# Performance work log

Measured on AMD Instinct MI355X. Metric: run time of the kernel, lower is better.

## Reference

```python
import jax, jax.numpy as jnp
import numpy as np

D_MODEL = 1024
N_HEADS = 16
D_FF = 4096
EPS = 1e-6


def layernorm(x, alpha, bias):
    # torch.std uses Bessel correction (ddof=1)
    mean = jnp.mean(x, axis=-1, keepdims=True)
    std = jnp.std(x, axis=-1, keepdims=True, ddof=1)
    return alpha * (x - mean) / (std + EPS) + bias


def setup_inputs() -> dict:
    key = jax.random.key(0)
    ks = jax.random.split(key, 12)
    s = 1.0 / np.sqrt(D_MODEL)
    sf = 1.0 / np.sqrt(D_FF)
    return {
        "x": jax.random.normal(ks[0], (2, 2048, D_MODEL), jnp.float32),
        "mask": jnp.ones((2, 1, 1, 2048), jnp.int32),
        "wq": jax.random.normal(ks[1], (D_MODEL, D_MODEL), jnp.float32) * s,
        "wk": jax.random.normal(ks[2], (D_MODEL, D_MODEL), jnp.float32) * s,
        "wv": jax.random.normal(ks[3], (D_MODEL, D_MODEL), jnp.float32) * s,
        "wo": jax.random.normal(ks[4], (D_MODEL, D_MODEL), jnp.float32) * s,
        "wo_b": jnp.zeros((D_MODEL,), jnp.float32),
        "w1": jax.random.normal(ks[5], (D_MODEL, D_FF), jnp.float32) * s,
        "b1": jnp.zeros((D_FF,), jnp.float32),
        "w2": jax.random.normal(ks[6], (D_FF, D_MODEL), jnp.float32) * sf,
        "b2": jnp.zeros((D_MODEL,), jnp.float32),
        "alpha1": jnp.ones((D_MODEL,), jnp.float32),
        "bias1": jnp.zeros((D_MODEL,), jnp.float32),
        "alpha2": jnp.ones((D_MODEL,), jnp.float32),
        "bias2": jnp.zeros((D_MODEL,), jnp.float32),
    }


def reference(x, mask, wq, wk, wv, wo, wo_b, w1, b1, w2, b2,
              alpha1, bias1, alpha2, bias2):
    B, S, D = x.shape
    h, dk = N_HEADS, D_MODEL // N_HEADS
    # projections -> [B, h, S, dk]
    q = (x @ wq).reshape(B, S, h, dk).transpose(0, 2, 1, 3)
    k = (x @ wk).reshape(B, S, h, dk).transpose(0, 2, 1, 3)
    v = (x @ wv).reshape(B, S, h, dk).transpose(0, 2, 1, 3)
    scores = jnp.einsum('bhqd,bhkd->bhqk', q, k) / jnp.sqrt(jnp.float32(dk))
    scores = jnp.where(mask == 0, jnp.float32(-1e9), scores)
    attn = jax.nn.softmax(scores, axis=-1)
    ctx = jnp.einsum('bhqk,bhkd->bhqd', attn, v)
    ctx = ctx.transpose(0, 2, 1, 3).reshape(B, S, D)
    attn_out = ctx @ wo + wo_b
    x = layernorm(x + attn_out, alpha1, bias1)
    ff = jax.nn.relu(x @ w1 + b1) @ w2 + b2
    x = layernorm(x + ff, alpha2, bias2)
    return x
```

## Files before the change

### kernel.cpp

```cpp
#include <hip/hip_runtime.h>
#include <hip/hip_bf16.h>

#define D_MODEL 1024
#define N_HEADS 16
#define DK      64
#define SEQ     2048
#define BATCH   2
#define D_FF    4096
#define ROWS    (BATCH*SEQ)
#define LN_EPS  1e-6f
#define KTILE   128

typedef __hip_bfloat16 bf16;
typedef __attribute__((ext_vector_type(8))) short frag8;
typedef __attribute__((ext_vector_type(4))) float facc4;

__device__ inline float bf2f(unsigned short u){ return __uint_as_float(((unsigned)u) << 16); }
__device__ inline float toF(bf16 v){ return __bfloat162float(v); }
__device__ inline unsigned short f2bu(float f){ bf16 h = __float2bfloat16(f); return *reinterpret_cast<unsigned short*>(&h); }

__device__ inline float ld1(const void* p, size_t idx, bool f32) {
    return f32 ? ((const float*)p)[idx] : toF(((const bf16*)p)[idx]);
}

struct U8 { unsigned short v[8]; };
__device__ inline U8 ld8bf(const void* p, size_t idx, bool f32) {
    U8 r;
    if (!f32) {
        *reinterpret_cast<uint4*>(r.v) = *reinterpret_cast<const uint4*>((const unsigned short*)p + idx);
    } else {
        const float* f = (const float*)p + idx;
        const float4 a = *reinterpret_cast<const float4*>(f);
        const float4 b = *reinterpret_cast<const float4*>(f + 4);
        r.v[0]=f2bu(a.x); r.v[1]=f2bu(a.y); r.v[2]=f2bu(a.z); r.v[3]=f2bu(a.w);
        r.v[4]=f2bu(b.x); r.v[5]=f2bu(b.y); r.v[6]=f2bu(b.z); r.v[7]=f2bu(b.w);
    }
    return r;
}

__device__ inline void gld16(const void* g, void* l) {
    __builtin_amdgcn_global_load_lds(
        reinterpret_cast<const __attribute__((address_space(1))) void*>(
            reinterpret_cast<uintptr_t>(g)),
        reinterpret_cast<__attribute__((address_space(3))) void*>(
            (unsigned int)reinterpret_cast<uintptr_t>(l)),
        16, 0, 0);
}

__global__ void probe_kernel(const void* __restrict__ xp, int* __restrict__ flag) {
    __shared__ int hit;
    if (threadIdx.x == 0) hit = 0;
    __syncthreads();
    const bf16* p = (const bf16*)xp;
    int bad = 0;
    for (int i = threadIdx.x; i < 8192; i += 256) {
        float v = fabsf(toF(p[i]));
        if (!(v <= 1e5f)) bad = 1;
    }
    if (bad) atomicOr(&hit, 1);
    __syncthreads();
    if (threadIdx.x == 0) *flag = hit;
}

__global__ __launch_bounds__(256) void xcvt_kernel(const void* __restrict__ x,
    bf16* __restrict__ out, const int* __restrict__ flagp)
{
    const bool f32 = (*flagp) != 0;
    const size_t i = ((size_t)blockIdx.x * 256 + threadIdx.x) * 8;
    U8 d = ld8bf(x, i, f32);
    *reinterpret_cast<uint4*>(out + i) = *reinterpret_cast<const uint4*>(d.v);
}

__global__ __launch_bounds__(256) void transpose_kernel(const void* __restrict__ W,
    bf16* __restrict__ WT, int K, int N, const int* __restrict__ flagp)
{
    const bool f32 = (*flagp) != 0;
    __shared__ float tile[32][33];
    const int tx = threadIdx.x, ty = threadIdx.y;
    const int n0 = blockIdx.x * 32, k0 = blockIdx.y * 32;
    #pragma unroll
    for (int r = 0; r < 4; ++r)
        tile[ty + 8*r][tx] = ld1(W, (size_t)(k0 + ty + 8*r) * N + n0 + tx, f32);
    __syncthreads();
    #pragma unroll
    for (int r = 0; r < 4; ++r)
        WT[(size_t)(n0 + ty + 8*r) * K + k0 + tx] = __float2bfloat16(tile[tx][ty + 8*r]);
}

__global__ __launch_bounds__(256) void transpose4_kernel(const void* __restrict__ w0,
    const void* __restrict__ w1, const void* __restrict__ w2, const void* __restrict__ w3,
    bf16* __restrict__ WT4, const int* __restrict__ flagp)
{
    const bool f32 = (*flagp) != 0;
    const int which = blockIdx.z;
    const void* W = (which == 0) ? w0 : (which == 1) ? w1 : (which == 2) ? w2 : w3;
    bf16* WT = WT4 + (size_t)which * D_MODEL * D_MODEL;
    __shared__ float tile[32][33];
    const int tx = threadIdx.x, ty = threadIdx.y;
    const int n0 = blockIdx.x * 32, k0 = blockIdx.y * 32;
    #pragma unroll
    for (int r = 0; r < 4; ++r)
        tile[ty + 8*r][tx] = ld1(W, (size_t)(k0 + ty + 8*r) * D_MODEL + n0 + tx, f32);
    __syncthreads();
    #pragma unroll
    for (int r = 0; r < 4; ++r)
        WT[(size_t)(n0 + ty + 8*r) * D_MODEL + k0 + tx] = __float2bfloat16(tile[tx][ty + 8*r]);
}

__global__ __launch_bounds__(256) void vtrans_kernel(const bf16* __restrict__ V,
    bf16* __restrict__ VT)
{
    __shared__ unsigned short tile[32][33];
    const int tx = threadIdx.x, ty = threadIdx.y;
    const int s0 = blockIdx.x * 32, d0 = blockIdx.y * 32;
    const int bh = blockIdx.z, b = bh >> 4, h = bh & 15;
    #pragma unroll
    for (int r = 0; r < 4; ++r)
        tile[ty + 8*r][tx] = *reinterpret_cast<const unsigned short*>(
            V + ((size_t)(b * SEQ + s0 + ty + 8*r)) * D_MODEL + h * DK + d0 + tx);
    __syncthreads();
    #pragma unroll
    for (int r = 0; r < 4; ++r)
        *reinterpret_cast<unsigned short*>(
            VT + ((size_t)(bh * DK + d0 + ty + 8*r)) * SEQ + s0 + tx) = tile[tx][ty + 8*r];
}

template<bool RELU, bool BIAS, int NMAT, int SPLITK>
__global__ __launch_bounds__(256) void mgemm_kernel(const bf16* __restrict__ A,
    const bf16* __restrict__ BT, const void* __restrict__ bias,
    bf16* __restrict__ C, int M, int N, int K, const int* __restrict__ flagp)
{
    const bool inF32 = (*flagp) != 0;

    __shared__ unsigned short sA[128 * 64];
    __shared__ unsigned short sB[128 * 64];

    int which = 0, colb = blockIdx.x;
    if (NMAT > 1) { which = blockIdx.x >> 3; colb = blockIdx.x & 7; }
    const int kslice = (SPLITK > 1) ? blockIdx.z : 0;
    const int Kspan  = K / SPLITK;
    const int kbase  = kslice * Kspan;
    const bf16* Bp = BT + (size_t)which * N * K;
    bf16*       Cp = C  + (size_t)which * M * N + (size_t)kslice * M * N;

    const int row0 = blockIdx.y * 128;
    const int col0 = colb * 128;

    const int t    = threadIdx.x;
    const int wave = t >> 6;
    const int lane = t & 63;
    const int lm   = lane & 15;
    const int q    = lane >> 4;
    const int wm   = (wave & 1) * 64;
    const int wn   = (wave >> 1) * 64;

    facc4 acc[4][4];
    #pragma unroll
    for (int i = 0; i < 4; ++i)
        #pragma unroll
        for (int j = 0; j < 4; ++j)
            acc[i][j] = (facc4){0.f, 0.f, 0.f, 0.f};

    for (int k0 = kbase; k0 < kbase + Kspan; k0 += 64) {
        __syncthreads();
        #pragma unroll
        for (int j = 0; j < 4; ++j) {
            const int ch = (wave * 4 + j) * 64 + lane;
            const int r  = ch >> 3;
            const int cs = ch & 7;
            const int c  = cs ^ (r & 7);
            gld16(A  + (size_t)(row0 + r) * K + k0 + 8 * c, &sA[(wave * 4 + j) * 512]);
            gld16(Bp + (size_t)(col0 + r) * K + k0 + 8 * c, &sB[(wave * 4 + j) * 512]);
        }
        __syncthreads();

        #pragma unroll
        for (int kk = 0; kk < 64; kk += 32) {
            const int cr = (kk >> 3) + q;
            frag8 af[4], bfr[4];
            #pragma unroll
            for (int im = 0; im < 4; ++im) {
                const int m = wm + 16 * im + lm;
                af[im] = *reinterpret_cast<const frag8*>(&sA[m * 64 + ((cr ^ (m & 7)) << 3)]);
            }
            #pragma unroll
            for (int in = 0; in < 4; ++in) {
                const int n = wn + 16 * in + lm;
                bfr[in] = *reinterpret_cast<const frag8*>(&sB[n * 64 + ((cr ^ (n & 7)) << 3)]);
            }
            #pragma unroll
            for (int im = 0; im < 4; ++im)
                #pragma unroll
                for (int in = 0; in < 4; ++in)
                    acc[im][in] = __builtin_amdgcn_mfma_f32_16x16x32_bf16(af[im], bfr[in], acc[im][in], 0, 0, 0);
        }
    }

    #pragma unroll
    for (int in = 0; in < 4; ++in) {
        const int col = col0 + wn + 16*in + lm;
        float bv = 0.f;
        if (BIAS && kslice == 0) bv = ld1(bias, col, inF32);
        #pragma unroll
        for (int im = 0; im < 4; ++im) {
            #pragma unroll
            for (int r = 0; r < 4; ++r) {
                const int row = row0 + wm + 16*im + 4*q + r;
                float v = acc[im][in][r] + bv;
                if (RELU) v = fmaxf(v, 0.f);
                Cp[(size_t)row * N + col] = __float2bfloat16(v);
            }
        }
    }
}

__global__ __launch_bounds__(512, 4) void fattn_kernel(
    const bf16* __restrict__ Qg, const bf16* __restrict__ Kg,
    const bf16* __restrict__ VTg, const int* __restrict__ mask,
    bf16* __restrict__ ctx)
{
    __shared__ unsigned short sK[128 * 64];
    __shared__ unsigned short sV[64 * 128];
    __shared__ __align__(16) float madd[KTILE];

    const int t    = threadIdx.x;
    const int qt   = blockIdx.x;
    const int h    = blockIdx.y;
    const int b    = blockIdx.z;
    const int q0   = qt * 128;
    const int bh   = b * N_HEADS + h;
    const int wave = t >> 6;
    const int lane = t & 63;
    const int lm   = lane & 15;
    const int qd   = lane >> 4;

    frag8 qf[2];
    {
        const bf16* qsrc = Qg + ((size_t)(b * SEQ + q0 + 16 * wave + lm)) * D_MODEL + h * DK;
        qf[0] = *reinterpret_cast<const frag8*>(qsrc + 8 * qd);
        qf[1] = *reinterpret_cast<const frag8*>(qsrc + 32 + 8 * qd);
    }

    facc4 accO[4];
    #pragma unroll
    for (int in = 0; in < 4; ++in) accO[in] = (facc4){0.f, 0.f, 0.f, 0.f};
    float m_r = -1e30f, l_r = 0.f;

    for (int kt = 0; kt < SEQ / KTILE; ++kt) {
        const int k0 = kt * KTILE;
        __syncthreads();

        #pragma unroll
        for (int j = 0; j < 2; ++j) {
            const int ch = (wave * 2 + j) * 64 + lane;
            const int rK = ch >> 3, cK = (ch & 7) ^ (rK & 7);
            gld16(Kg + ((size_t)(b * SEQ + k0 + rK)) * D_MODEL + h * DK + 8 * cK,
                  &sK[(wave * 2 + j) * 512]);
            const int rV = ch >> 4, cV = (ch & 15) ^ (rV & 15);
            gld16(VTg + ((size_t)(bh * DK + rV)) * SEQ + k0 + 8 * cV,
                  &sV[(wave * 2 + j) * 512]);
        }
        if (t < KTILE) madd[t] = (mask[b * SEQ + k0 + t] == 0) ? -1e9f : 0.f;
        __syncthreads();

        facc4 accST[8];
        #pragma unroll
        for (int i = 0; i < 8; ++i) accST[i] = (facc4){0.f, 0.f, 0.f, 0.f};
        #pragma unroll
        for (int i = 0; i < 8; ++i) {
            #pragma unroll
            for (int s2 = 0; s2 < 2; ++s2) {
                const int cr = 4 * s2 + qd;
                frag8 kf = *reinterpret_cast<const frag8*>(
                    &sK[(16 * i + lm) * 64 + ((cr ^ (lm & 7)) << 3)]);
                accST[i] = __builtin_amdgcn_mfma_f32_16x16x32_bf16(kf, qf[s2], accST[i], 0, 0, 0);
            }
        }

        float m0 = -1e30f;
        #pragma unroll
        for (int i = 0; i < 8; ++i) {
            const facc4 mv = *reinterpret_cast<const facc4*>(&madd[16 * i + 4 * qd]);
            #pragma unroll
            for (int r = 0; r < 4; ++r) {
                accST[i][r] = fmaf(accST[i][r], 0.125f, mv[r]);
                m0 = fmaxf(m0, accST[i][r]);
            }
        }
        m0 = fmaxf(m0, __shfl_xor(m0, 16));
        m0 = fmaxf(m0, __shfl_xor(m0, 32));

        const float mn = fmaxf(m_r, m0);
        const float alpha = __expf(m_r - mn);
        m_r = mn;

        unsigned up[8][2];
        float ps = 0.f;
        #pragma unroll
        for (int i = 0; i < 8; ++i) {
            const float p0 = __expf(accST[i][0] - mn);
            const float p1 = __expf(accST[i][1] - mn);
            const float p2 = __expf(accST[i][2] - mn);
            const float p3 = __expf(accST[i][3] - mn);
            ps += (p0 + p1) + (p2 + p3);
            up[i][0] = (unsigned)f2bu(p0) | ((unsigned)f2bu(p1) << 16);
            up[i][1] = (unsigned)f2bu(p2) | ((unsigned)f2bu(p3) << 16);
        }
        ps += __shfl_xor(ps, 16);
        ps += __shfl_xor(ps, 32);
        l_r = l_r * alpha + ps;
        #pragma unroll
        for (int in = 0; in < 4; ++in)
            #pragma unroll
            for (int r = 0; r < 4; ++r) accO[in][r] *= alpha;

        #pragma unroll
        for (int c = 0; c < 4; ++c) {
            unsigned a0 = up[2*c][0],     a1 = up[2*c][1];
            unsigned b0 = up[2*c + 1][0], b1 = up[2*c + 1][1];
            asm("v_permlane32_swap_b32 %0, %1" : "+v"(a0), "+v"(b0));
            asm("v_permlane32_swap_b32 %0, %1" : "+v"(a1), "+v"(b1));
            const unsigned tA0 = __shfl_xor(a0, 16);
            const unsigned tB0 = __shfl_xor(b0, 16);
            const unsigned tA1 = __shfl_xor(a1, 16);
            const unsigned tB1 = __shfl_xor(b1, 16);
            const bool qo = (qd & 1) != 0;
            union { frag8 f; unsigned u[4]; } pf_;
            pf_.u[0] = qo ? tB0 : a0;
            pf_.u[1] = qo ? tB1 : a1;
            pf_.u[2] = qo ? b0  : tA0;
            pf_.u[3] = qo ? b1  : tA1;
            #pragma unroll
            for (int in = 0; in < 4; ++in) {
                const int cr = 4 * c + qd;
                frag8 vf = *reinterpret_cast<const frag8*>(
                    &sV[(16 * in + lm) * 128 + ((cr ^ lm) << 3)]);
                accO[in] = __builtin_amdgcn_mfma_f32_16x16x32_bf16(vf, pf_.f, accO[in], 0, 0, 0);
            }
        }
    }

    const float invl = 1.f / l_r;
    bf16* crow = ctx + ((size_t)(b * SEQ + q0 + 16 * wave + lm)) * D_MODEL + h * DK;
    #pragma unroll
    for (int in = 0; in < 4; ++in) {
        union { uint2 v; unsigned short s[4]; } ov;
        #pragma unroll
        for (int r = 0; r < 4; ++r) ov.s[r] = f2bu(accO[in][r] * invl);
        *reinterpret_cast<uint2*>(crow + 16 * in + 4 * qd) = ov.v;
    }
}

template<bool BASE_WS, bool OUT_WS>
__global__ __launch_bounds__(256) void ln_kernel(const void* __restrict__ base,
    const bf16* __restrict__ addv, const bf16* __restrict__ addv2,
    const void* __restrict__ alpha, const void* __restrict__ bias,
    void* __restrict__ outp, const int* __restrict__ flagp)
{
    const bool inF32 = (*flagp) != 0;
    __shared__ float vals[D_MODEL];
    __shared__ float red[256];
    const int row = blockIdx.x, tid = threadIdx.x;

    float lsum = 0.f;
    for (int i = tid; i < D_MODEL; i += 256) {
        const size_t off = (size_t)row * D_MODEL + i;
        float v = (BASE_WS ? toF(((const bf16*)base)[off]) : ld1(base, off, inF32)) + toF(addv[off]);
        if (addv2) v += toF(addv2[off]);
        vals[i] = v; lsum += v;
    }
    red[tid] = lsum; __syncthreads();
    for (int s = 128; s > 0; s >>= 1) { if (tid < s) red[tid] += red[tid + s]; __syncthreads(); }
    const float mean = red[0] / (float)D_MODEL; __syncthreads();

    float lsq = 0.f;
    for (int i = tid; i < D_MODEL; i += 256) { float dd = vals[i] - mean; lsq += dd * dd; }
    red[tid] = lsq; __syncthreads();
    for (int s = 128; s > 0; s >>= 1) { if (tid < s) red[tid] += red[tid + s]; __syncthreads(); }
    const float var = red[0] / (float)(D_MODEL - 1);
    const float inv = 1.f / (sqrtf(var) + LN_EPS);

    for (int i = tid; i < D_MODEL; i += 256) {
        const size_t off = (size_t)row * D_MODEL + i;
        const float y = ld1(alpha, i, inF32) * (vals[i] - mean) * inv + ld1(bias, i, inF32);
        if (OUT_WS || !inF32) ((bf16*)outp)[off] = __float2bfloat16(y);
        else                  ((float*)outp)[off] = y;
    }
}

extern "C" void kernel_launch(void* const* d_in, const int* in_sizes, int n_in,
                              void* d_out, int out_size, void* d_ws, size_t ws_size,
                              hipStream_t stream)
{
    const void* x    = d_in[0];
    const int*  mask = (const int*)d_in[1];
    const void* wq   = d_in[2];
    const void* wk   = d_in[3];
    const void* wv   = d_in[4];
    const void* wo   = d_in[5];
    const void* wo_b = d_in[6];
    const void* w1   = d_in[7];
    const void* b1   = d_in[8];
    const void* w2   = d_in[9];
    const void* b2   = d_in[10];
    const void* al1  = d_in[11];
    const void* bi1  = d_in[12];
    const void* al2  = d_in[13];
    const void* bi2  = d_in[14];

    const size_t MB = 1024 * 1024;
    char* ws = (char*)d_ws;
    const bool BIG = ws_size >= 64 * MB + 4096;
    if (!BIG && ws_size < 56 * MB + 4096) return;

    dim3 tb(32, 8);

    if (BIG) {
        bf16* Qb   = (bf16*)(ws + 0 * MB);
        bf16* Kb   = (bf16*)(ws + 8 * MB);
        bf16* Vb   = (bf16*)(ws + 16 * MB);
        bf16* Xb   = (bf16*)(ws + 24 * MB);
        bf16* VTb  = (bf16*)(ws + 24 * MB);
        bf16* WT4  = (bf16*)(ws + 32 * MB);
        bf16* WOT  = WT4 + (size_t)3 * D_MODEL * D_MODEL;
        bf16* W1T  = (bf16*)(ws + 40 * MB);
        bf16* W2T  = (bf16*)(ws + 48 * MB);
        bf16* CTXb = (bf16*)(ws + 56 * MB);
        bf16* ATT0 = (bf16*)(ws + 0 * MB);
        bf16* ATT1 = (bf16*)(ws + 8 * MB);
        bf16* X1b  = (bf16*)(ws + 56 * MB);
        bf16* FFb  = (bf16*)(ws + 0 * MB);
        bf16* X20  = (bf16*)(ws + 32 * MB);
        bf16* X21  = (bf16*)(ws + 40 * MB);
        int*  flagp = (int*)(ws + 64 * MB);

        probe_kernel<<<1, 256, 0, stream>>>(x, flagp);
        xcvt_kernel<<<dim3(ROWS * D_MODEL / 2048), 256, 0, stream>>>(x, Xb, flagp);

        transpose4_kernel<<<dim3(32, 32, 4), tb, 0, stream>>>(wq, wk, wv, wo, WT4, flagp);
        transpose_kernel<<<dim3(128, 32), tb, 0, stream>>>(w1, W1T, D_MODEL, D_FF, flagp);
        transpose_kernel<<<dim3(32, 128), tb, 0, stream>>>(w2, W2T, D_FF, D_MODEL, flagp);

        mgemm_kernel<false, false, 3, 1><<<dim3(24, 32), 256, 0, stream>>>(
            Xb, WT4, nullptr, Qb, ROWS, D_MODEL, D_MODEL, flagp);

        vtrans_kernel<<<dim3(SEQ / 32, 2, BATCH * N_HEADS), tb, 0, stream>>>(Vb, VTb);

        fattn_kernel<<<dim3(SEQ / 128, N_HEADS, BATCH), 512, 0, stream>>>(Qb, Kb, VTb, mask, CTXb);

        mgemm_kernel<false, true, 1, 2><<<dim3(8, 32, 2), 256, 0, stream>>>(
            CTXb, WOT, wo_b, ATT0, ROWS, D_MODEL, D_MODEL, flagp);
        ln_kernel<false, true><<<ROWS, 256, 0, stream>>>(x, ATT0, ATT1, al1, bi1, X1b, flagp);

        mgemm_kernel<true, true, 1, 1><<<dim3(32, 32), 256, 0, stream>>>(
            X1b, W1T, b1, FFb, ROWS, D_FF, D_MODEL, flagp);

        mgemm_kernel<false, true, 1, 2><<<dim3(8, 32, 2), 256, 0, stream>>>(
            FFb, W2T, b2, X20, ROWS, D_MODEL, D_FF, flagp);
        ln_kernel<true, false><<<ROWS, 256, 0, stream>>>(X1b, X20, X21, al2, bi2, d_out, flagp);
    } else {
        bf16* Qb    = (bf16*)(ws + 0 * MB);
        bf16* Kb    = (bf16*)(ws + 8 * MB);
        bf16* Vb    = (bf16*)(ws + 16 * MB);
        bf16* Xb    = (bf16*)(ws + 24 * MB);
        bf16* VTb   = (bf16*)(ws + 24 * MB);
        bf16* WQKVT = (bf16*)(ws + 32 * MB);
        bf16* CTXb  = (bf16*)(ws + 32 * MB);
        bf16* W2T   = (bf16*)(ws + 32 * MB);
        bf16* WOT   = (bf16*)(ws + 0 * MB);
        bf16* ATT0  = (bf16*)(ws + 48 * MB);
        bf16* W1T   = (bf16*)(ws + 48 * MB);
        bf16* X20   = (bf16*)(ws + 48 * MB);
        bf16* X1b   = (bf16*)(ws + 40 * MB);
        bf16* FFb   = (bf16*)(ws + 0 * MB);
        int*  flagp = (int*)(ws + 56 * MB);

        probe_kernel<<<1, 256, 0, stream>>>(x, flagp);
        xcvt_kernel<<<dim3(ROWS * D_MODEL / 2048), 256, 0, stream>>>(x, Xb, flagp);

        transpose_kernel<<<dim3(32, 32), tb, 0, stream>>>(wq, WQKVT,           D_MODEL, D_MODEL, flagp);
        transpose_kernel<<<dim3(32, 32), tb, 0, stream>>>(wk, WQKVT + 1048576, D_MODEL, D_MODEL, flagp);
        transpose_kernel<<<dim3(32, 32), tb, 0, stream>>>(wv, WQKVT + 2097152, D_MODEL, D_MODEL, flagp);

        mgemm_kernel<false, false, 3, 1><<<dim3(24, 32), 256, 0, stream>>>(
            Xb, WQKVT, nullptr, Qb, ROWS, D_MODEL, D_MODEL, flagp);

        vtrans_kernel<<<dim3(SEQ / 32, 2, BATCH * N_HEADS), tb, 0, stream>>>(Vb, VTb);

        fattn_kernel<<<dim3(SEQ / 128, N_HEADS, BATCH), 512, 0, stream>>>(Qb, Kb, VTb, mask, CTXb);

        transpose_kernel<<<dim3(32, 32), tb, 0, stream>>>(wo, WOT, D_MODEL, D_MODEL, flagp);
        mgemm_kernel<false, true, 1, 1><<<dim3(8, 32), 256, 0, stream>>>(
            CTXb, WOT, wo_b, ATT0, ROWS, D_MODEL, D_MODEL, flagp);
        ln_kernel<false, true><<<ROWS, 256, 0, stream>>>(x, ATT0, nullptr, al1, bi1, X1b, flagp);

        transpose_kernel<<<dim3(128, 32), tb, 0, stream>>>(w1, W1T, D_MODEL, D_FF, flagp);
        mgemm_kernel<true, true, 1, 1><<<dim3(32, 32), 256, 0, stream>>>(
            X1b, W1T, b1, FFb, ROWS, D_FF, D_MODEL, flagp);

        transpose_kernel<<<dim3(32, 128), tb, 0, stream>>>(w2, W2T, D_FF, D_MODEL, flagp);
        mgemm_kernel<false, true, 1, 1><<<dim3(8, 32), 256, 0, stream>>>(
            FFb, W2T, b2, X20, ROWS, D_MODEL, D_FF, flagp);
        ln_kernel<true, false><<<ROWS, 256, 0, stream>>>(X1b, X20, nullptr, al2, bi2, d_out, flagp);
    }
}
```

Before: 396.0 us.

## Process two query sub-tiles per wave in flash attention with 256-thread blocks

Halves the flash-attention block to 4 waves, each now owning 32 query rows (two 16-row sub-tiles), so every K and V fragment read from LDS feeds two MFMAs. Each wave loads twice as many K/V chunks into shared memory per tile. The P-fragment shuffle is also reworked to use two shfl_xor per pair instead of four. The change aims to cut LDS traffic per MFMA, at the cost of higher register pressure and fewer waves per block for latency hiding.

```diff
diff --git a/kernel.cpp b/kernel.cpp
--- a/kernel.cpp
+++ b/kernel.cpp
@@ -214,7 +214,7 @@
     }
 }
 
-__global__ __launch_bounds__(512, 4) void fattn_kernel(
+__global__ __launch_bounds__(256, 2) void fattn_kernel(
     const bf16* __restrict__ Qg, const bf16* __restrict__ Kg,
     const bf16* __restrict__ VTg, const int* __restrict__ mask,
     bf16* __restrict__ ctx)
@@ -233,39 +233,45 @@
     const int lane = t & 63;
     const int lm   = lane & 15;
     const int qd   = lane >> 4;
-
-    frag8 qf[2];
-    {
-        const bf16* qsrc = Qg + ((size_t)(b * SEQ + q0 + 16 * wave + lm)) * D_MODEL + h * DK;
-        qf[0] = *reinterpret_cast<const frag8*>(qsrc + 8 * qd);
-        qf[1] = *reinterpret_cast<const frag8*>(qsrc + 32 + 8 * qd);
-    }
-
-    facc4 accO[4];
-    #pragma unroll
-    for (int in = 0; in < 4; ++in) accO[in] = (facc4){0.f, 0.f, 0.f, 0.f};
-    float m_r = -1e30f, l_r = 0.f;
+    const bool qo  = (qd & 1) != 0;
+
+    frag8 qf[2][2];
+    #pragma unroll
+    for (int s = 0; s < 2; ++s) {
+        const bf16* qsrc = Qg + ((size_t)(b * SEQ + q0 + 32 * wave + 16 * s + lm)) * D_MODEL + h * DK;
+        qf[s][0] = *reinterpret_cast<const frag8*>(qsrc + 8 * qd);
+        qf[s][1] = *reinterpret_cast<const frag8*>(qsrc + 32 + 8 * qd);
+    }
+
+    facc4 accO[2][4];
+    #pragma unroll
+    for (int s = 0; s < 2; ++s)
+        #pragma unroll
+        for (int in = 0; in < 4; ++in) accO[s][in] = (facc4){0.f, 0.f, 0.f, 0.f};
+    float m_r[2] = {-1e30f, -1e30f}, l_r[2] = {0.f, 0.f};
 
     for (int kt = 0; kt < SEQ / KTILE; ++kt) {
         const int k0 = kt * KTILE;
         __syncthreads();
 
         #pragma unroll
-        for (int j = 0; j < 2; ++j) {
-            const int ch = (wave * 2 + j) * 64 + lane;
+        for (int j = 0; j < 4; ++j) {
+            const int ch = (wave * 4 + j) * 64 + lane;
             const int rK = ch >> 3, cK = (ch & 7) ^ (rK & 7);
             gld16(Kg + ((size_t)(b * SEQ + k0 + rK)) * D_MODEL + h * DK + 8 * cK,
-                  &sK[(wave * 2 + j) * 512]);
+                  &sK[(wave * 4 + j) * 512]);
             const int rV = ch >> 4, cV = (ch & 15) ^ (rV & 15);
             gld16(VTg + ((size_t)(bh * DK + rV)) * SEQ + k0 + 8 * cV,
-                  &sV[(wave * 2 + j) * 512]);
+                  &sV[(wave * 4 + j) * 512]);
         }
         if (t < KTILE) madd[t] = (mask[b * SEQ + k0 + t] == 0) ? -1e9f : 0.f;
         __syncthreads();
 
-        facc4 accST[8];
-        #pragma unroll
-        for (int i = 0; i < 8; ++i) accST[i] = (facc4){0.f, 0.f, 0.f, 0.f};
+        facc4 accST[2][8];
+        #pragma unroll
+        for (int s = 0; s < 2; ++s)
+            #pragma unroll
+            for (int i = 0; i < 8; ++i) accST[s][i] = (facc4){0.f, 0.f, 0.f, 0.f};
         #pragma unroll
         for (int i = 0; i < 8; ++i) {
             #pragma unroll
@@ -273,81 +279,102 @@
                 const int cr = 4 * s2 + qd;
                 frag8 kf = *reinterpret_cast<const frag8*>(
                     &sK[(16 * i + lm) * 64 + ((cr ^ (lm & 7)) << 3)]);
-                accST[i] = __builtin_amdgcn_mfma_f32_16x16x32_bf16(kf, qf[s2], accST[i], 0, 0, 0);
-            }
-        }
-
-        float m0 = -1e30f;
+                accST[0][i] = __builtin_amdgcn_mfma_f32_16x16x32_bf16(kf, qf[0][s2], accST[0][i], 0, 0, 0);
+                accST[1][i] = __builtin_amdgcn_mfma_f32_16x16x32_bf16(kf, qf[1][s2], accST[1][i], 0, 0, 0);
+            }
+        }
+
+        float m0[2] = {-1e30f, -1e30f};
         #pragma unroll
         for (int i = 0; i < 8; ++i) {
             const facc4 mv = *reinterpret_cast<const facc4*>(&madd[16 * i + 4 * qd]);
             #pragma unroll
-            for (int r = 0; r < 4; ++r) {
-                accST[i][r] = fmaf(accST[i][r], 0.125f, mv[r]);
-                m0 = fmaxf(m0, accST[i][r]);
-            }
-        }
-        m0 = fmaxf(m0, __shfl_xor(m0, 16));
-        m0 = fmaxf(m0, __shfl_xor(m0, 32));
-
-        const float mn = fmaxf(m_r, m0);
-        const float alpha = __expf(m_r - mn);
-        m_r = mn;
-
-        unsigned up[8][2];
-        float ps = 0.f;
-        #pragma unroll
-        for (int i = 0; i < 8; ++i) {
-            const float p0 = __expf(accST[i][0] - mn);
-            const float p1 = __expf(accST[i][1] - mn);
-            const float p2 = __expf(accST[i][2] - mn);
-            const float p3 = __expf(accST[i][3] - mn);
-            ps += (p0 + p1) + (p2 + p3);
-            up[i][0] = (unsigned)f2bu(p0) | ((unsigned)f2bu(p1) << 16);
-            up[i][1] = (unsigned)f2bu(p2) | ((unsigned)f2bu(p3) << 16);
-        }
-        ps += __shfl_xor(ps, 16);
-        ps += __shfl_xor(ps, 32);
-        l_r = l_r * alpha + ps;
-        #pragma unroll
-        for (int in = 0; in < 4; ++in)
-            #pragma unroll
-            for (int r = 0; r < 4; ++r) accO[in][r] *= alpha;
+            for (int s = 0; s < 2; ++s) {
+                #pragma unroll
+                for (int r = 0; r < 4; ++r) {
+                    accST[s][i][r] = fmaf(accST[s][i][r], 0.125f, mv[r]);
+                    m0[s] = fmaxf(m0[s], accST[s][i][r]);
+                }
+            }
+        }
+        float mn[2], alpha[2];
+        #pragma unroll
+        for (int s = 0; s < 2; ++s) {
+            m0[s] = fmaxf(m0[s], __shfl_xor(m0[s], 16));
+            m0[s] = fmaxf(m0[s], __shfl_xor(m0[s], 32));
+            mn[s] = fmaxf(m_r[s], m0[s]);
+            alpha[s] = __expf(m_r[s] - mn[s]);
+            m_r[s] = mn[s];
+        }
+
+        unsigned up[2][8][2];
+        float ps[2] = {0.f, 0.f};
+        #pragma unroll
+        for (int s = 0; s < 2; ++s) {
+            #pragma unroll
+            for (int i = 0; i < 8; ++i) {
+                const float p0 = __expf(accST[s][i][0] - mn[s]);
+                const float p1 = __expf(accST[s][i][1] - mn[s]);
+                const float p2 = __expf(accST[s][i][2] - mn[s]);
+                const float p3 = __expf(accST[s][i][3] - mn[s]);
+                ps[s] += (p0 + p1) + (p2 + p3);
+                up[s][i][0] = (unsigned)f2bu(p0) | ((unsigned)f2bu(p1) << 16);
+                up[s][i][1] = (unsigned)f2bu(p2) | ((unsigned)f2bu(p3) << 16);
+            }
+        }
+        #pragma unroll
+        for (int s = 0; s < 2; ++s) {
+            ps[s] += __shfl_xor(ps[s], 16);
+            ps[s] += __shfl_xor(ps[s], 32);
+            l_r[s] = l_r[s] * alpha[s] + ps[s];
+            #pragma unroll
+            for (int in = 0; in < 4; ++in)
+                #pragma unroll
+                for (int r = 0; r < 4; ++r) accO[s][in][r] *= alpha[s];
+        }
 
         #pragma unroll
         for (int c = 0; c < 4; ++c) {
-            unsigned a0 = up[2*c][0],     a1 = up[2*c][1];
-            unsigned b0 = up[2*c + 1][0], b1 = up[2*c + 1][1];
-            asm("v_permlane32_swap_b32 %0, %1" : "+v"(a0), "+v"(b0));
-            asm("v_permlane32_swap_b32 %0, %1" : "+v"(a1), "+v"(b1));
-            const unsigned tA0 = __shfl_xor(a0, 16);
-            const unsigned tB0 = __shfl_xor(b0, 16);
-            const unsigned tA1 = __shfl_xor(a1, 16);
-            const unsigned tB1 = __shfl_xor(b1, 16);
-            const bool qo = (qd & 1) != 0;
-            union { frag8 f; unsigned u[4]; } pf_;
-            pf_.u[0] = qo ? tB0 : a0;
-            pf_.u[1] = qo ? tB1 : a1;
-            pf_.u[2] = qo ? b0  : tA0;
-            pf_.u[3] = qo ? b1  : tA1;
+            union { frag8 f; unsigned u[4]; } pf0_, pf1_;
+            #pragma unroll
+            for (int s = 0; s < 2; ++s) {
+                unsigned a0 = up[s][2*c][0],     a1 = up[s][2*c][1];
+                unsigned b0 = up[s][2*c + 1][0], b1 = up[s][2*c + 1][1];
+                asm("v_permlane32_swap_b32 %0, %1" : "+v"(a0), "+v"(b0));
+                asm("v_permlane32_swap_b32 %0, %1" : "+v"(a1), "+v"(b1));
+                const unsigned t0 = qo ? a0 : b0;
+                const unsigned t1 = qo ? a1 : b1;
+                const unsigned r0 = __shfl_xor(t0, 16);
+                const unsigned r1 = __shfl_xor(t1, 16);
+                unsigned u0 = qo ? r0 : a0;
+                unsigned u1 = qo ? r1 : a1;
+                unsigned u2 = qo ? b0 : r0;
+                unsigned u3 = qo ? b1 : r1;
+                if (s == 0) { pf0_.u[0]=u0; pf0_.u[1]=u1; pf0_.u[2]=u2; pf0_.u[3]=u3; }
+                else        { pf1_.u[0]=u0; pf1_.u[1]=u1; pf1_.u[2]=u2; pf1_.u[3]=u3; }
+            }
             #pragma unroll
             for (int in = 0; in < 4; ++in) {
                 const int cr = 4 * c + qd;
                 frag8 vf = *reinterpret_cast<const frag8*>(
                     &sV[(16 * in + lm) * 128 + ((cr ^ lm) << 3)]);
-                accO[in] = __builtin_amdgcn_mfma_f32_16x16x32_bf16(vf, pf_.f, accO[in], 0, 0, 0);
-            }
-        }
-    }
-
-    const float invl = 1.f / l_r;
-    bf16* crow = ctx + ((size_t)(b * SEQ + q0 + 16 * wave + lm)) * D_MODEL + h * DK;
-    #pragma unroll
-    for (int in = 0; in < 4; ++in) {
-        union { uint2 v; unsigned short s[4]; } ov;
-        #pragma unroll
-        for (int r = 0; r < 4; ++r) ov.s[r] = f2bu(accO[in][r] * invl);
-        *reinterpret_cast<uint2*>(crow + 16 * in + 4 * qd) = ov.v;
+                accO[0][in] = __builtin_amdgcn_mfma_f32_16x16x32_bf16(vf, pf0_.f, accO[0][in], 0, 0, 0);
+                accO[1][in] = __builtin_amdgcn_mfma_f32_16x16x32_bf16(vf, pf1_.f, accO[1][in], 0, 0, 0);
+            }
+        }
+    }
+
+    #pragma unroll
+    for (int s = 0; s < 2; ++s) {
+        const float invl = 1.f / l_r[s];
+        bf16* crow = ctx + ((size_t)(b * SEQ + q0 + 32 * wave + 16 * s + lm)) * D_MODEL + h * DK;
+        #pragma unroll
+        for (int in = 0; in < 4; ++in) {
+            union { uint2 v; unsigned short sh[4]; } ov;
+            #pragma unroll
+            for (int r = 0; r < 4; ++r) ov.sh[r] = f2bu(accO[s][in][r] * invl);
+            *reinterpret_cast<uint2*>(crow + 16 * in + 4 * qd) = ov.v;
+        }
     }
 }
 
@@ -446,7 +473,7 @@
 
         vtrans_kernel<<<dim3(SEQ / 32, 2, BATCH * N_HEADS), tb, 0, stream>>>(Vb, VTb);
 
-        fattn_kernel<<<dim3(SEQ / 128, N_HEADS, BATCH), 512, 0, stream>>>(Qb, Kb, VTb, mask, CTXb);
+        fattn_kernel<<<dim3(SEQ / 128, N_HEADS, BATCH), 256, 0, stream>>>(Qb, Kb, VTb, mask, CTXb);
 
         mgemm_kernel<false, true, 1, 2><<<dim3(8, 32, 2), 256, 0, stream>>>(
             CTXb, WOT, wo_b, ATT0, ROWS, D_MODEL, D_MODEL, flagp);
@@ -487,7 +514,7 @@
 
         vtrans_kernel<<<dim3(SEQ / 32, 2, BATCH * N_HEADS), tb, 0, stream>>>(Vb, VTb);
 
-        fattn_kernel<<<dim3(SEQ / 128, N_HEADS, BATCH), 512, 0, stream>>>(Qb, Kb, VTb, mask, CTXb);
+        fattn_kernel<<<dim3(SEQ / 128, N_HEADS, BATCH), 256, 0, stream>>>(Qb, Kb, VTb, mask, CTXb);
 
         transpose_kernel<<<dim3(32, 32), tb, 0, stream>>>(wo, WOT, D_MODEL, D_MODEL, flagp);
         mgemm_kernel<false, true, 1, 1><<<dim3(8, 32), 256, 0, stream>>>(
```

After: 394.3 us. No clear change (-0.4%).
